# Kernel optimization log

Measured on AMD Instinct MI355X. Metric: run time of the kernel, lower is better.

Reference implementation:

```python
import jax, jax.numpy as jnp
import numpy as np

F_IN = 128
H = 512


def _uniform(key, shape, stdv):
    return jax.random.uniform(key, shape, jnp.float32, -stdv, stdv)


def setup_inputs() -> dict:
    key = jax.random.key(0)
    ks = jax.random.split(key, 20)
    B, T, F = 512, 96, F_IN
    x = jax.random.normal(ks[0], (B, T, F), jnp.float32)
    mask = jax.random.randint(ks[1], (B, T, F), 0, 2).astype(jnp.int32)
    sH = 1.0 / np.sqrt(H)
    sF = 1.0 / np.sqrt(F)
    inp = {
        'x': x,
        'mask': mask,
        # TemporalDecay h: W [H, F], b [H]
        'Wdh': _uniform(ks[2], (H, F), sH), 'bdh': _uniform(ks[3], (H,), sH),
        # TemporalDecay x (diag): W [F, F], b [F]
        'Wdx': _uniform(ks[4], (F, F), sF), 'bdx': _uniform(ks[5], (F,), sF),
        # hist_reg Linear(H, F)
        'Wh': _uniform(ks[6], (F, H), sH), 'bh': _uniform(ks[7], (F,), sH),
        # feat_reg: W [F, F] (off-diagonal mask), b [F]
        'Wf': _uniform(ks[8], (F, F), sF), 'bf': _uniform(ks[9], (F,), sF),
        # weight_combine Linear(2F, F)
        'Wc': _uniform(ks[10], (F, 2 * F), 1.0 / np.sqrt(2 * F)),
        'bc': _uniform(ks[11], (F,), 1.0 / np.sqrt(2 * F)),
        # LSTMCell(2F, H): torch gate order i, f, g, o
        'Wih': _uniform(ks[12], (4 * H, 2 * F), sH),
        'Whh': _uniform(ks[13], (4 * H, H), sH),
        'bih': _uniform(ks[14], (4 * H,), sH),
        'bhh': _uniform(ks[15], (4 * H,), sH),
    }
    return inp


def _rits_forward(x, m, Wdh, bdh, Wdx, bdx, Wh, bh, Wf, bf, Wc, bc, Wih, Whh, bih, bhh):
    B, T, F = x.shape
    eye = jnp.eye(F, dtype=x.dtype)
    Wf_m = Wf * (1.0 - eye)
    Wdx_m = Wdx * eye         # diagonal TemporalDecay

    # compute_delta (freq=1): delta[0]=0; delta[i]=m[i-1]+ (1-m[i-1])*(delta[i-1]+1)
    m_tm = jnp.swapaxes(m, 0, 1)  # [T, B, F]
    def dstep(prev, mp):
        nxt = mp + (1.0 - mp) * (prev + 1.0)
        return nxt, nxt
    _, drest = jax.lax.scan(dstep, jnp.zeros((B, F), x.dtype), m_tm[:-1])
    delta_tm = jnp.concatenate([jnp.zeros((1, B, F), x.dtype), drest], axis=0)

    x_tm = jnp.swapaxes(x, 0, 1)  # [T, B, F]

    def step(carry, inp):
        h, c = carry
        x_s, m_s, d = inp
        gamma_h = jnp.exp(-jax.nn.relu(d @ Wdh.T + bdh))          # [B, H]
        x_h = h @ Wh.T + bh                                        # [B, F]
        x_c = m_s * x_s + (1.0 - m_s) * x_h
        h = h * gamma_h
        z_h = x_c @ Wf_m.T + bf
        gamma_x = jnp.exp(-jax.nn.relu(d @ Wdx_m.T + bdx))
        alpha = jax.nn.sigmoid(jnp.concatenate([gamma_x, m_s], axis=1) @ Wc.T + bc)
        c_h = alpha * z_h + (1.0 - alpha) * x_h
        c_c = m_s * x_s + (1.0 - m_s) * c_h
        inputs = jnp.concatenate([c_c, m_s], axis=1)               # [B, 2F]
        gates = inputs @ Wih.T + bih + h @ Whh.T + bhh             # [B, 4H]
        i_g, f_g, g_g, o_g = jnp.split(gates, 4, axis=1)
        c = jax.nn.sigmoid(f_g) * c + jax.nn.sigmoid(i_g) * jnp.tanh(g_g)
        h = jax.nn.sigmoid(o_g) * jnp.tanh(c)
        return (h, c), (c_c, c_h, z_h, x_h)

    h0 = jnp.zeros((B, H), x.dtype)
    c0 = jnp.zeros((B, H), x.dtype)
    _, (c_c, c_h, z_h, x_h) = jax.lax.scan(step, (h0, c0), (x_tm, m_tm, delta_tm))
    # back to [B, T, F]
    tr = lambda a: jnp.swapaxes(a, 0, 1)
    return tr(c_c), tr(c_h), tr(z_h), tr(x_h)


def reference(x, mask, Wdh, bdh, Wdx, bdx, Wh, bh, Wf, bf, Wc, bc, Wih, Whh, bih, bhh):
    m = mask.astype(x.dtype)
    imputation, c_h, z_h, x_h = _rits_forward(
        x, m, Wdh, bdh, Wdx, bdx, Wh, bh, Wf, bf, Wc, bc, Wih, Whh, bih, bhh)
    return (imputation, (c_h, z_h, x_h))
```

## Files before the change

### kernel.cpp

```cpp
#include <hip/hip_runtime.h>
#include <cstdint>
#include <cstddef>

#define BB 512
#define TT 96
#define FF 128
#define HH 512
#define BTF 6291456
#define BH  262144

typedef unsigned short ushort_t;
typedef __attribute__((ext_vector_type(8))) short bf16x8;
typedef __attribute__((ext_vector_type(4))) float f32x4;

static constexpr size_t OFF_FLAGS = 0;
static constexpr size_t OFF_WDXD  = 2048;
static constexpr size_t OFF_DELTA = 4096;
static constexpr size_t OFF_MBF   = OFF_DELTA + 12582912;
static constexpr size_t OFF_ALPHA = OFF_MBF   + 12582912;
static constexpr size_t OFF_GH    = OFF_ALPHA + 12582912;
static constexpr size_t OFF_H     = OFF_GH    + 50331648;
static constexpr size_t OFF_HDEC  = OFF_H     + 2097152;
static constexpr size_t OFF_CCBF  = OFF_HDEC  + 1048576;

static constexpr int LDS_W     = 0;
static constexpr int LDS_GATES = 98304;
static constexpr int LDS_BIAS  = 133120;
static constexpr int LDS_XPART = 133376;
static constexpr int LDS_XC    = 141568;
static constexpr int LDS_TOTAL = 142592;

__device__ __forceinline__ float bf2f(ushort_t u) {
  union { unsigned u; float f; } c; c.u = ((unsigned)u) << 16; return c.f;
}
__device__ __forceinline__ ushort_t f2bf(float f) {
  union { float f; unsigned u; } c; c.f = f;
  unsigned x = c.u;
  unsigned r = (x + 0x7FFFu + ((x >> 16) & 1u)) >> 16;
  return (ushort_t)r;
}
__device__ __forceinline__ float lo2f(unsigned p) {
  union { unsigned u; float f; } c; c.u = p << 16; return c.f;
}
__device__ __forceinline__ float hi2f(unsigned p) {
  union { unsigned u; float f; } c; c.u = p & 0xffff0000u; return c.f;
}
__device__ __forceinline__ float sigm(float v) { return 1.0f / (1.0f + __expf(-v)); }

__device__ __forceinline__ bf16x8 cload16(const ushort_t* p) {
  union { unsigned long long q[2]; bf16x8 v; } u;
  unsigned long long* a = (unsigned long long*)p;
  u.q[0] = __hip_atomic_load(a,     __ATOMIC_RELAXED, __HIP_MEMORY_SCOPE_AGENT);
  u.q[1] = __hip_atomic_load(a + 1, __ATOMIC_RELAXED, __HIP_MEMORY_SCOPE_AGENT);
  return u.v;
}
__device__ __forceinline__ float cloadf(const float* p) {
  unsigned v = __hip_atomic_load((const unsigned*)p, __ATOMIC_RELAXED, __HIP_MEMORY_SCOPE_AGENT);
  union { unsigned u; float f; } c; c.u = v; return c.f;
}
__device__ __forceinline__ void cstore8(void* p, unsigned long long v) {
  __hip_atomic_store((unsigned long long*)p, v, __ATOMIC_RELAXED, __HIP_MEMORY_SCOPE_AGENT);
}
__device__ __forceinline__ void cstore4(void* p, unsigned v) {
  __hip_atomic_store((unsigned*)p, v, __ATOMIC_RELAXED, __HIP_MEMORY_SCOPE_AGENT);
}
__device__ __forceinline__ void cstore2(ushort_t* p, ushort_t v) {
  __hip_atomic_store(p, v, __ATOMIC_RELAXED, __HIP_MEMORY_SCOPE_AGENT);
}
__device__ __forceinline__ float rdlane_f(float v, int sl) {
  return __int_as_float(__builtin_amdgcn_readlane(__float_as_int(v), sl));
}

__global__ void k_cvt(const float* __restrict__ Wdx, char* __restrict__ ws) {
  int tid = threadIdx.x;
  unsigned* fl = (unsigned*)(ws + OFF_FLAGS);
  fl[tid] = 0; fl[256 + tid] = 0;
  float* wdxd = (float*)(ws + OFF_WDXD);
  if (tid < FF) wdxd[tid] = Wdx[tid * (FF + 1)];
}

__global__ void k_prep(const int* __restrict__ mask, char* __restrict__ ws) {
  ushort_t* delta = (ushort_t*)(ws + OFF_DELTA);
  ushort_t* mbf   = (ushort_t*)(ws + OFF_MBF);
  int gtid = blockIdx.x * 256 + threadIdx.x;
  int b = gtid >> 7, f = gtid & 127;
  const int* mrow = mask + (size_t)b * (TT * FF) + f;
  float dprev = 0.0f;
  for (int t = 0; t < TT; ++t) {
    float d;
    if (t == 0) d = 0.0f;
    else {
      int mp = mrow[(t - 1) * FF];
      d = mp ? 1.0f : dprev + 1.0f;
    }
    dprev = d;
    delta[((size_t)t * BB + b) * FF + f] = f2bf(d);
    int mc = mrow[t * FF];
    mbf[(size_t)b * (TT * FF) + t * FF + f] = f2bf((float)mc);
  }
}

__global__ __launch_bounds__(256, 4) void k_gh(const float* __restrict__ Wdh,
                                               const float* __restrict__ bdh,
                                               char* __restrict__ ws) {
  __shared__ ushort_t A_lds[64 * 136];
  __shared__ ushort_t B_lds[64 * 136];
  const ushort_t* delta = (const ushort_t*)(ws + OFF_DELTA);
  ushort_t* gh = (ushort_t*)(ws + OFF_GH);
  int tid = threadIdx.x;
  int m0 = blockIdx.x * 64;
  int n0 = blockIdx.y * 64;
  for (int v = tid; v < 1024; v += 256) {
    int row = v >> 4, seg = v & 15;
    *(uint4*)&A_lds[row * 136 + seg * 8] =
        *(const uint4*)(delta + ((size_t)(m0 + row)) * FF + seg * 8);
  }
  for (int v = tid; v < 1024; v += 256) {
    int n = v >> 4, seg = v & 15;
    const float* src = Wdh + (size_t)(n0 + n) * FF + seg * 8;
    ushort_t tmp[8];
#pragma unroll
    for (int j = 0; j < 8; ++j) tmp[j] = f2bf(src[j]);
    *(uint4*)&B_lds[n * 136 + seg * 8] = *(const uint4*)tmp;
  }
  __syncthreads();
  int wave = tid >> 6, lane = tid & 63, quad = lane >> 4, lan = lane & 15;
  int mt = wave;
  f32x4 acc[4];
#pragma unroll
  for (int nt = 0; nt < 4; ++nt) acc[nt] = (f32x4){0.f, 0.f, 0.f, 0.f};
  const ushort_t* ab = &A_lds[(mt * 16 + lan) * 136 + quad * 8];
#pragma unroll
  for (int kk = 0; kk < 4; ++kk) {
    bf16x8 af = *(const bf16x8*)(ab + kk * 32);
#pragma unroll
    for (int nt = 0; nt < 4; ++nt) {
      bf16x8 bfv = *(const bf16x8*)(&B_lds[(nt * 16 + lan) * 136 + kk * 32 + quad * 8]);
      acc[nt] = __builtin_amdgcn_mfma_f32_16x16x32_bf16(af, bfv, acc[nt], 0, 0, 0);
    }
  }
#pragma unroll
  for (int nt = 0; nt < 4; ++nt) {
#pragma unroll
    for (int r = 0; r < 4; ++r) {
      int mg = m0 + mt * 16 + quad * 4 + r;
      int nc = n0 + nt * 16 + lan;
      float v = acc[nt][r] + bdh[nc];
      gh[(size_t)mg * HH + nc] = f2bf(__expf(-fmaxf(v, 0.0f)));
    }
  }
}

__global__ __launch_bounds__(256, 4) void k_al(const float* __restrict__ Wc,
                                               const float* __restrict__ bc,
                                               const float* __restrict__ bdx,
                                               char* __restrict__ ws) {
  __shared__ ushort_t A_lds[64 * 136];
  __shared__ ushort_t B_lds[64 * 136];
  const ushort_t* delta = (const ushort_t*)(ws + OFF_DELTA);
  const ushort_t* mbf   = (const ushort_t*)(ws + OFF_MBF);
  const float* wdxd     = (const float*)(ws + OFF_WDXD);
  ushort_t* alpha = (ushort_t*)(ws + OFF_ALPHA);
  int tid = threadIdx.x;
  int m0 = blockIdx.x * 64;
  int n0 = blockIdx.y * 64;
  int wave = tid >> 6, lane = tid & 63, quad = lane >> 4, lan = lane & 15;
  int mt = wave;
  f32x4 acc[4];
#pragma unroll
  for (int nt = 0; nt < 4; ++nt) acc[nt] = (f32x4){0.f, 0.f, 0.f, 0.f};
  for (int c = 0; c < 2; ++c) {
    __syncthreads();
    if (c == 0) {
      for (int v = tid; v < 1024; v += 256) {
        int row = v >> 4, seg = v & 15;
        int mg = m0 + row;
        ushort_t tmp[8];
#pragma unroll
        for (int j = 0; j < 8; ++j) {
          int k = seg * 8 + j;
          float d = bf2f(delta[(size_t)mg * FF + k]);
          float g = __expf(-fmaxf(fmaf(d, wdxd[k], bdx[k]), 0.0f));
          tmp[j] = f2bf(g);
        }
        *(uint4*)&A_lds[row * 136 + seg * 8] = *(const uint4*)tmp;
      }
    } else {
      for (int v = tid; v < 1024; v += 256) {
        int row = v >> 4, seg = v & 15;
        int mg = m0 + row;
        int t = mg >> 9, b = mg & 511;
        *(uint4*)&A_lds[row * 136 + seg * 8] =
            *(const uint4*)(mbf + ((size_t)b * TT + t) * FF + seg * 8);
      }
    }
    for (int v = tid; v < 1024; v += 256) {
      int n = v >> 4, seg = v & 15;
      const float* src = Wc + (size_t)(n0 + n) * 256 + c * 128 + seg * 8;
      ushort_t tmp[8];
#pragma unroll
      for (int j = 0; j < 8; ++j) tmp[j] = f2bf(src[j]);
      *(uint4*)&B_lds[n * 136 + seg * 8] = *(const uint4*)tmp;
    }
    __syncthreads();
    const ushort_t* ab = &A_lds[(mt * 16 + lan) * 136 + quad * 8];
#pragma unroll
    for (int kk = 0; kk < 4; ++kk) {
      bf16x8 af = *(const bf16x8*)(ab + kk * 32);
#pragma unroll
      for (int nt = 0; nt < 4; ++nt) {
        bf16x8 bfv = *(const bf16x8*)(&B_lds[(nt * 16 + lan) * 136 + kk * 32 + quad * 8]);
        acc[nt] = __builtin_amdgcn_mfma_f32_16x16x32_bf16(af, bfv, acc[nt], 0, 0, 0);
      }
    }
  }
#pragma unroll
  for (int nt = 0; nt < 4; ++nt) {
#pragma unroll
    for (int r = 0; r < 4; ++r) {
      int mg = m0 + mt * 16 + quad * 4 + r;
      int nc = n0 + nt * 16 + lan;
      float v = acc[nt][r] + bc[nc];
      alpha[(size_t)mg * FF + nc] = f2bf(sigm(v));
    }
  }
}

__device__ __forceinline__ void bar_arrive(unsigned* cnt) {
  __syncthreads();
  if (threadIdx.x == 0)
    __hip_atomic_fetch_add(cnt, 1u, __ATOMIC_RELAXED, __HIP_MEMORY_SCOPE_AGENT);
}
__device__ __forceinline__ void bar_wait(unsigned* cnt, unsigned target) {
  if (threadIdx.x == 0) {
    while (__hip_atomic_load(cnt, __ATOMIC_RELAXED, __HIP_MEMORY_SCOPE_AGENT) < target)
      __builtin_amdgcn_s_sleep(1);
  }
  __syncthreads();
}
__device__ __forceinline__ void bar_wait_wave(unsigned* cnt, unsigned target, int lane) {
  if (lane == 0) {
    while (__hip_atomic_load(cnt, __ATOMIC_RELAXED, __HIP_MEMORY_SCOPE_AGENT) < target)
      __builtin_amdgcn_s_sleep(1);
  }
  asm volatile("" ::: "memory");
}

__global__ __launch_bounds__(512, 2) void k_main(
    const float* __restrict__ x, const int* __restrict__ mask,
    const float* __restrict__ Wh, const float* __restrict__ Wf,
    const float* __restrict__ bh, const float* __restrict__ bfr,
    const float* __restrict__ Wih, const float* __restrict__ Whh,
    const float* __restrict__ bih, const float* __restrict__ bhh,
    float* __restrict__ out, char* __restrict__ ws) {
  extern __shared__ char smem[];
  ushort_t* W_fr     = (ushort_t*)(smem + LDS_W);
  float* gates_lds   = (float*)(smem + LDS_GATES);
  float* bias_lds    = (float*)(smem + LDS_BIAS);
  float* xh_part     = (float*)(smem + LDS_XPART);
  float* xc_s        = (float*)(smem + LDS_XC);

  unsigned* cnts = (unsigned*)(ws + OFF_FLAGS);
  const ushort_t* alpha = (const ushort_t*)(ws + OFF_ALPHA);
  const ushort_t* gh    = (const ushort_t*)(ws + OFF_GH);
  const ushort_t* mbf   = (const ushort_t*)(ws + OFF_MBF);
  float*    hws  = (float*)(ws + OFF_H);
  ushort_t* hdws = (ushort_t*)(ws + OFF_HDEC);
  ushort_t* ccbf = (ushort_t*)(ws + OFF_CCBF);

  const int tid  = threadIdx.x;
  const int wg   = blockIdx.x;
  const int g    = wg & 7;
  const int mwg  = wg >> 3;
  const int ng   = mwg;
  const int wave = tid >> 6, lane = tid & 63, quad = lane >> 4, lan = lane & 15;
  const int mt = wave & 3, khalf = wave >> 2;
  const int r0 = g * 64 + mwg * 2;
  const int arow = g * 64 + mt * 16 + lan;

  unsigned* cntA = cnts + (g * 2 + 0) * 32;
  unsigned* cntB = cnts + (g * 2 + 1) * 32;

  for (int q = tid; q < 6144; q += 512) {
    int sec = q >> 10, rem = q & 1023;
    int f = rem >> 6, lw = rem & 63;
    int nt = f >> 2, kk = f & 3;
    int lan_ = lw & 15, quad_ = lw >> 4;
    int r = nt * 512 + ng * 16 + lan_;
    const float* src = (sec < 2)
        ? (Wih + (size_t)r * 256 + sec * 128 + kk * 32 + quad_ * 8)
        : (Whh + (size_t)r * 512 + (sec - 2) * 128 + kk * 32 + quad_ * 8);
    float4 v0 = *(const float4*)src;
    float4 v1 = *(const float4*)(src + 4);
    ushort_t t8[8] = { f2bf(v0.x), f2bf(v0.y), f2bf(v0.z), f2bf(v0.w),
                       f2bf(v1.x), f2bf(v1.y), f2bf(v1.z), f2bf(v1.w) };
    *(uint4*)&W_fr[q * 8] = *(const uint4*)t8;
  }
  if (tid < 64) {
    int r = (tid >> 4) * 512 + ng * 16 + (tid & 15);
    bias_lds[tid] = bih[r] + bhh[r];
  }

#define WFRAG(sec, nt, kk) (*(const bf16x8*)&W_fr[((((sec) * 16 + (nt) * 4 + (kk)) * 64 + lane)) * 8])

  unsigned wh_p[64];
  {
    const float* s0 = Wh + (size_t)lane * HH + 64 * wave;
    const float* s1 = Wh + (size_t)(lane + 64) * HH + 64 * wave;
#pragma unroll
    for (int i4 = 0; i4 < 16; ++i4) {
      float4 a = *(const float4*)(s0 + i4 * 4);
      float4 b = *(const float4*)(s1 + i4 * 4);
      wh_p[i4 * 4 + 0] = ((unsigned)f2bf(a.x)) | (((unsigned)f2bf(b.x)) << 16);
      wh_p[i4 * 4 + 1] = ((unsigned)f2bf(a.y)) | (((unsigned)f2bf(b.y)) << 16);
      wh_p[i4 * 4 + 2] = ((unsigned)f2bf(a.z)) | (((unsigned)f2bf(b.z)) << 16);
      wh_p[i4 * 4 + 3] = ((unsigned)f2bf(a.w)) | (((unsigned)f2bf(b.w)) << 16);
    }
  }
  unsigned wf_p[16];
  {
    const float* s0 = Wf + (size_t)lane * FF + 16 * wave;
    const float* s1 = Wf + (size_t)(lane + 64) * FF + 16 * wave;
#pragma unroll
    for (int i4 = 0; i4 < 4; ++i4) {
      float4 a = *(const float4*)(s0 + i4 * 4);
      float4 b = *(const float4*)(s1 + i4 * 4);
      wf_p[i4 * 4 + 0] = ((unsigned)f2bf(a.x)) | (((unsigned)f2bf(b.x)) << 16);
      wf_p[i4 * 4 + 1] = ((unsigned)f2bf(a.y)) | (((unsigned)f2bf(b.y)) << 16);
      wf_p[i4 * 4 + 2] = ((unsigned)f2bf(a.z)) | (((unsigned)f2bf(b.z)) << 16);
      wf_p[i4 * 4 + 3] = ((unsigned)f2bf(a.w)) | (((unsigned)f2bf(b.w)) << 16);
    }
  }
  const int fdot = tid & 127;
  float bh_r = 0.f, bfr_r = 0.f, wfd_r = 0.f;
  if (tid < 256) {
    bh_r  = bh[fdot];
    bfr_r = bfr[fdot];
    wfd_r = bf2f(f2bf(Wf[(size_t)fdot * FF + fdot]));
  }

  const int b_l = tid >> 3, jl0 = 2 * (tid & 7);
  const int bglob = g * 64 + b_l, j0 = ng * 16 + jl0;
  cstore8(&hws[(size_t)bglob * HH + j0], 0ull);
  cstore4(&hdws[(size_t)bglob * HH + j0], 0u);
  float c_r0 = 0.f, c_r1 = 0.f;

  unsigned epA = 0, epB = 1;
  bar_arrive(cntB);

  for (int t = 0; t < TT; ++t) {
    float xv = 0.f, mv = 0.f, al = 0.f;
    if (tid < 256) {
      int bl = tid >> 7;
      int b = r0 + bl;
      size_t gix = (size_t)b * (TT * FF) + (size_t)t * FF + fdot;
      xv = x[gix];
      mv = (float)mask[gix];
      al = bf2f(alpha[((size_t)t * BB + b) * FF + fdot]);
    }
    unsigned gh2 = 0;
    if (t < TT - 1)
      gh2 = *(const unsigned*)&gh[((size_t)(t + 1) * BB + bglob) * HH + j0];
    bf16x8 A0[4], A1[4], A2[4];
    if (khalf == 0) {
      const ushort_t* mrow = mbf + ((size_t)arow * TT + t) * FF + quad * 8;
#pragma unroll
      for (int kk = 0; kk < 4; ++kk) A0[kk] = *(const bf16x8*)(mrow + kk * 32);
    }

    bar_wait(cntB, 32u * epB);

    const float* hbuf = hws + (size_t)(t & 1) * BH;
    float h0r = cloadf(hbuf + (size_t)r0 * HH + 64 * wave + lane);
    float h1r = cloadf(hbuf + (size_t)(r0 + 1) * HH + 64 * wave + lane);
    {
      const ushort_t* hdec = hdws + (size_t)(t & 1) * BH;
      const ushort_t* hrow = hdec + (size_t)arow * HH + quad * 8;
      if (khalf == 0) {
#pragma unroll
        for (int kk = 0; kk < 4; ++kk) A1[kk] = cload16(hrow + kk * 32);
#pragma unroll
        for (int kk = 0; kk < 4; ++kk) A2[kk] = cload16(hrow + 128 + kk * 32);
      } else {
#pragma unroll
        for (int kk = 0; kk < 4; ++kk) A0[kk] = cload16(hrow + 256 + kk * 32);
#pragma unroll
        for (int kk = 0; kk < 4; ++kk) A1[kk] = cload16(hrow + 384 + kk * 32);
      }
    }

    f32x4 acc[4];
#pragma unroll
    for (int nt = 0; nt < 4; ++nt) acc[nt] = (f32x4){0.f, 0.f, 0.f, 0.f};
    if (khalf == 0) {
#pragma unroll
      for (int kk = 0; kk < 4; ++kk)
#pragma unroll
        for (int nt = 0; nt < 4; ++nt)
          acc[nt] = __builtin_amdgcn_mfma_f32_16x16x32_bf16(A0[kk], WFRAG(1, nt, kk), acc[nt], 0, 0, 0);
#pragma unroll
      for (int kk = 0; kk < 4; ++kk)
#pragma unroll
        for (int nt = 0; nt < 4; ++nt)
          acc[nt] = __builtin_amdgcn_mfma_f32_16x16x32_bf16(A1[kk], WFRAG(2, nt, kk), acc[nt], 0, 0, 0);
#pragma unroll
      for (int kk = 0; kk < 4; ++kk)
#pragma unroll
        for (int nt = 0; nt < 4; ++nt)
          acc[nt] = __builtin_amdgcn_mfma_f32_16x16x32_bf16(A2[kk], WFRAG(3, nt, kk), acc[nt], 0, 0, 0);
    } else {
#pragma unroll
      for (int kk = 0; kk < 4; ++kk)
#pragma unroll
        for (int nt = 0; nt < 4; ++nt)
          acc[nt] = __builtin_amdgcn_mfma_f32_16x16x32_bf16(A0[kk], WFRAG(4, nt, kk), acc[nt], 0, 0, 0);
#pragma unroll
      for (int kk = 0; kk < 4; ++kk)
#pragma unroll
        for (int nt = 0; nt < 4; ++nt)
          acc[nt] = __builtin_amdgcn_mfma_f32_16x16x32_bf16(A1[kk], WFRAG(5, nt, kk), acc[nt], 0, 0, 0);
#pragma unroll
      for (int nt = 0; nt < 4; ++nt)
#pragma unroll
        for (int r = 0; r < 4; ++r)
          gates_lds[(64 + mt * 16 + quad * 4 + r) * 68 + nt * 16 + lan] = acc[nt][r];
    }

    {
      float a00 = 0.f, a01 = 0.f, a10 = 0.f, a11 = 0.f;
#pragma unroll
      for (int k = 0; k < 64; ++k) {
        float hk0 = rdlane_f(h0r, k);
        float hk1 = rdlane_f(h1r, k);
        unsigned wp = wh_p[k];
        float w0 = lo2f(wp), w1 = hi2f(wp);
        a00 = fmaf(w0, hk0, a00);
        a10 = fmaf(w1, hk0, a10);
        a01 = fmaf(w0, hk1, a01);
        a11 = fmaf(w1, hk1, a11);
      }
      xh_part[(wave * 2 + 0) * 128 + lane]      = a00;
      xh_part[(wave * 2 + 0) * 128 + 64 + lane] = a10;
      xh_part[(wave * 2 + 1) * 128 + lane]      = a01;
      xh_part[(wave * 2 + 1) * 128 + 64 + lane] = a11;
    }
    __syncthreads();

    float xh_r = 0.f;
    if (tid < 256) {
      int bl = tid >> 7;
      float s = bh_r;
#pragma unroll
      for (int w2 = 0; w2 < 8; ++w2) s += xh_part[(w2 * 2 + bl) * 128 + fdot];
      xh_r = s;
      float xcv = fmaf(1.0f - mv, xh_r, mv * xv);
      xc_s[bl * 128 + fdot] = xcv;
    }
    __syncthreads();

    {
      float z00 = 0.f, z01 = 0.f, z10 = 0.f, z11 = 0.f;
      float x0 = xc_s[16 * wave + (lane & 15)];
      float x1 = xc_s[128 + 16 * wave + (lane & 15)];
#pragma unroll
      for (int k = 0; k < 16; ++k) {
        float xk0 = rdlane_f(x0, k);
        float xk1 = rdlane_f(x1, k);
        unsigned wp = wf_p[k];
        float w0 = lo2f(wp), w1 = hi2f(wp);
        z00 = fmaf(w0, xk0, z00);
        z10 = fmaf(w1, xk0, z10);
        z01 = fmaf(w0, xk1, z01);
        z11 = fmaf(w1, xk1, z11);
      }
      xh_part[(wave * 2 + 0) * 128 + lane]      = z00;
      xh_part[(wave * 2 + 0) * 128 + 64 + lane] = z10;
      xh_part[(wave * 2 + 1) * 128 + lane]      = z01;
      xh_part[(wave * 2 + 1) * 128 + 64 + lane] = z11;
    }
    __syncthreads();

    float zh = 0.f, ch = 0.f, cc = 0.f;
    if (tid < 256) {
      int bl = tid >> 7;
      int b = r0 + bl;
      float xcv = xc_s[bl * 128 + fdot];
      float s = bfr_r - xcv * wfd_r;
#pragma unroll
      for (int w2 = 0; w2 < 8; ++w2) s += xh_part[(w2 * 2 + bl) * 128 + fdot];
      zh = s;
      ch = fmaf(al, zh, (1.0f - al) * xh_r);
      cc = fmaf(1.0f - mv, ch, mv * xv);
      cstore2(&ccbf[b * FF + fdot], f2bf(cc));
    }

    bar_arrive(cntA); ++epA;

    if (tid < 256) {
      int bl = tid >> 7;
      int b = r0 + bl;
      size_t ob = (size_t)b * (TT * FF) + (size_t)t * FF + fdot;
      out[ob] = cc;
      out[BTF + ob] = ch;
      out[2 * (size_t)BTF + ob] = zh;
      out[3 * (size_t)BTF + ob] = xh_r;
    }

    if (khalf == 0) {
      bar_wait_wave(cntA, 32u * epA, lane);
      const ushort_t* ccrow = ccbf + (size_t)arow * FF + quad * 8;
      bf16x8 AC[4];
#pragma unroll
      for (int kk = 0; kk < 4; ++kk) AC[kk] = cload16(ccrow + kk * 32);
#pragma unroll
      for (int kk = 0; kk < 4; ++kk) {
#pragma unroll
        for (int nt = 0; nt < 4; ++nt) {
          acc[nt] = __builtin_amdgcn_mfma_f32_16x16x32_bf16(AC[kk], WFRAG(0, nt, kk), acc[nt], 0, 0, 0);
        }
      }
#pragma unroll
      for (int nt = 0; nt < 4; ++nt)
#pragma unroll
        for (int r = 0; r < 4; ++r)
          gates_lds[(mt * 16 + quad * 4 + r) * 68 + nt * 16 + lan] = acc[nt][r];
    }
    __syncthreads();

    {
      const float* g0 = &gates_lds[(size_t)b_l * 68 + jl0];
      const float* g1 = &gates_lds[(size_t)(64 + b_l) * 68 + jl0];
      float2 gI = make_float2(g0[0] + g1[0] + bias_lds[jl0],
                              g0[1] + g1[1] + bias_lds[jl0 + 1]);
      float2 gF = make_float2(g0[16] + g1[16] + bias_lds[16 + jl0],
                              g0[17] + g1[17] + bias_lds[16 + jl0 + 1]);
      float2 gG = make_float2(g0[32] + g1[32] + bias_lds[32 + jl0],
                              g0[33] + g1[33] + bias_lds[32 + jl0 + 1]);
      float2 gO = make_float2(g0[48] + g1[48] + bias_lds[48 + jl0],
                              g0[49] + g1[49] + bias_lds[48 + jl0 + 1]);
      c_r0 = fmaf(sigm(gF.x), c_r0, sigm(gI.x) * tanhf(gG.x));
      c_r1 = fmaf(sigm(gF.y), c_r1, sigm(gI.y) * tanhf(gG.y));
      float h0 = sigm(gO.x) * tanhf(c_r0);
      float h1 = sigm(gO.y) * tanhf(c_r1);
      float* hwN = hws + (size_t)((t + 1) & 1) * BH;
      ushort_t* hdN = hdws + (size_t)((t + 1) & 1) * BH;
      union { float2 f; unsigned long long q; } hu; hu.f = make_float2(h0, h1);
      cstore8(&hwN[(size_t)bglob * HH + j0], hu.q);
      float gHa = lo2f(gh2), gHb = hi2f(gh2);
      unsigned hp = ((unsigned)f2bf(h0 * gHa)) | (((unsigned)f2bf(h1 * gHb)) << 16);
      cstore4(&hdN[(size_t)bglob * HH + j0], hp);
    }

    bar_arrive(cntB); ++epB;
  }
#undef WFRAG
}

extern "C" void kernel_launch(void* const* d_in, const int* in_sizes, int n_in,
                              void* d_out, int out_size, void* d_ws, size_t ws_size,
                              hipStream_t stream) {
  (void)in_sizes; (void)n_in; (void)out_size; (void)ws_size;
  const float* x   = (const float*)d_in[0];
  const int*   mask= (const int*)d_in[1];
  const float* Wdh = (const float*)d_in[2];
  const float* bdh = (const float*)d_in[3];
  const float* Wdx = (const float*)d_in[4];
  const float* bdx = (const float*)d_in[5];
  const float* Wh  = (const float*)d_in[6];
  const float* bh  = (const float*)d_in[7];
  const float* Wf  = (const float*)d_in[8];
  const float* bfr = (const float*)d_in[9];
  const float* Wc  = (const float*)d_in[10];
  const float* bc  = (const float*)d_in[11];
  const float* Wih = (const float*)d_in[12];
  const float* Whh = (const float*)d_in[13];
  const float* bih = (const float*)d_in[14];
  const float* bhh = (const float*)d_in[15];
  float* out = (float*)d_out;
  char* ws = (char*)d_ws;

  hipLaunchKernelGGL(k_cvt,  dim3(1),   dim3(256), 0, stream, Wdx, ws);
  hipLaunchKernelGGL(k_prep, dim3(256), dim3(256), 0, stream, mask, ws);
  hipLaunchKernelGGL(k_gh,   dim3(768, 8), dim3(256), 0, stream, Wdh, bdh, ws);
  hipLaunchKernelGGL(k_al,   dim3(768, 2), dim3(256), 0, stream, Wc, bc, bdx, ws);

  hipFuncSetAttribute((const void*)k_main, hipFuncAttributeMaxDynamicSharedMemorySize, LDS_TOTAL);
  void* args[] = { (void*)&x, (void*)&mask, (void*)&Wh, (void*)&Wf, (void*)&bh, (void*)&bfr,
                   (void*)&Wih, (void*)&Whh, (void*)&bih, (void*)&bhh, (void*)&out, (void*)&ws };
  hipLaunchCooperativeKernel((const void*)k_main, dim3(256), dim3(512), args, LDS_TOTAL, stream);
}
```

Measured before the change: 1.516 ms.

## Map workgroup groups to XCCs and use L2-coherent sc0 loads for shared state

```diff
diff --git a/kernel.cpp b/kernel.cpp
--- a/kernel.cpp
+++ b/kernel.cpp
@@ -28,7 +28,8 @@
 static constexpr int LDS_BIAS  = 133120;
 static constexpr int LDS_XPART = 133376;
 static constexpr int LDS_XC    = 141568;
-static constexpr int LDS_TOTAL = 142592;
+static constexpr int LDS_MISC  = 142592;
+static constexpr int LDS_TOTAL = 142608;
 
 __device__ __forceinline__ float bf2f(ushort_t u) {
   union { unsigned u; float f; } c; c.u = ((unsigned)u) << 16; return c.f;
@@ -47,25 +48,19 @@
 }
 __device__ __forceinline__ float sigm(float v) { return 1.0f / (1.0f + __expf(-v)); }
 
-__device__ __forceinline__ bf16x8 cload16(const ushort_t* p) {
-  union { unsigned long long q[2]; bf16x8 v; } u;
-  unsigned long long* a = (unsigned long long*)p;
-  u.q[0] = __hip_atomic_load(a,     __ATOMIC_RELAXED, __HIP_MEMORY_SCOPE_AGENT);
-  u.q[1] = __hip_atomic_load(a + 1, __ATOMIC_RELAXED, __HIP_MEMORY_SCOPE_AGENT);
-  return u.v;
-}
-__device__ __forceinline__ float cloadf(const float* p) {
-  unsigned v = __hip_atomic_load((const unsigned*)p, __ATOMIC_RELAXED, __HIP_MEMORY_SCOPE_AGENT);
-  union { unsigned u; float f; } c; c.u = v; return c.f;
-}
-__device__ __forceinline__ void cstore8(void* p, unsigned long long v) {
-  __hip_atomic_store((unsigned long long*)p, v, __ATOMIC_RELAXED, __HIP_MEMORY_SCOPE_AGENT);
-}
-__device__ __forceinline__ void cstore4(void* p, unsigned v) {
-  __hip_atomic_store((unsigned*)p, v, __ATOMIC_RELAXED, __HIP_MEMORY_SCOPE_AGENT);
-}
-__device__ __forceinline__ void cstore2(ushort_t* p, ushort_t v) {
-  __hip_atomic_store(p, v, __ATOMIC_RELAXED, __HIP_MEMORY_SCOPE_AGENT);
+__device__ __forceinline__ bf16x8 ld16_l2(const ushort_t* p) {
+  bf16x8 r;
+  asm volatile("global_load_dwordx4 %0, %1, off sc0" : "=v"(r) : "v"(p));
+  return r;
+}
+__device__ __forceinline__ float ldf_l2(const float* p) {
+  float r;
+  asm volatile("global_load_dword %0, %1, off sc0" : "=v"(r) : "v"(p));
+  return r;
+}
+__device__ __forceinline__ void waitvm0() {
+  asm volatile("s_waitcnt vmcnt(0)" ::: "memory");
+  __builtin_amdgcn_sched_barrier(0);
 }
 __device__ __forceinline__ float rdlane_f(float v, int sl) {
   return __int_as_float(__builtin_amdgcn_readlane(__float_as_int(v), sl));
@@ -259,6 +254,7 @@
   float* bias_lds    = (float*)(smem + LDS_BIAS);
   float* xh_part     = (float*)(smem + LDS_XPART);
   float* xc_s        = (float*)(smem + LDS_XC);
+  int*   misc        = (int*)(smem + LDS_MISC);
 
   unsigned* cnts = (unsigned*)(ws + OFF_FLAGS);
   const ushort_t* alpha = (const ushort_t*)(ws + OFF_ALPHA);
@@ -268,10 +264,18 @@
   ushort_t* hdws = (ushort_t*)(ws + OFF_HDEC);
   ushort_t* ccbf = (ushort_t*)(ws + OFF_CCBF);
 
-  const int tid  = threadIdx.x;
-  const int wg   = blockIdx.x;
-  const int g    = wg & 7;
-  const int mwg  = wg >> 3;
+  const int tid = threadIdx.x;
+
+  unsigned xcc;
+  asm("s_getreg_b32 %0, hwreg(HW_REG_XCC_ID)" : "=s"(xcc));
+  const int g = (int)(xcc & 7u);
+  if (tid == 0) {
+    unsigned s = __hip_atomic_fetch_add(cnts + g * 64 + 16, 1u, __ATOMIC_RELAXED,
+                                        __HIP_MEMORY_SCOPE_AGENT);
+    misc[0] = (int)(s & 31u);
+  }
+  __syncthreads();
+  const int mwg  = misc[0];
   const int ng   = mwg;
   const int wave = tid >> 6, lane = tid & 63, quad = lane >> 4, lan = lane & 15;
   const int mt = wave & 3, khalf = wave >> 2;
@@ -341,8 +345,8 @@
 
   const int b_l = tid >> 3, jl0 = 2 * (tid & 7);
   const int bglob = g * 64 + b_l, j0 = ng * 16 + jl0;
-  cstore8(&hws[(size_t)bglob * HH + j0], 0ull);
-  cstore4(&hdws[(size_t)bglob * HH + j0], 0u);
+  *(float2*)&hws[(size_t)bglob * HH + j0] = make_float2(0.f, 0.f);
+  *(unsigned*)&hdws[(size_t)bglob * HH + j0] = 0u;
   float c_r0 = 0.f, c_r1 = 0.f;
 
   unsigned epA = 0, epB = 1;
@@ -371,23 +375,24 @@
     bar_wait(cntB, 32u * epB);
 
     const float* hbuf = hws + (size_t)(t & 1) * BH;
-    float h0r = cloadf(hbuf + (size_t)r0 * HH + 64 * wave + lane);
-    float h1r = cloadf(hbuf + (size_t)(r0 + 1) * HH + 64 * wave + lane);
+    float h0r = ldf_l2(hbuf + (size_t)r0 * HH + 64 * wave + lane);
+    float h1r = ldf_l2(hbuf + (size_t)(r0 + 1) * HH + 64 * wave + lane);
     {
       const ushort_t* hdec = hdws + (size_t)(t & 1) * BH;
       const ushort_t* hrow = hdec + (size_t)arow * HH + quad * 8;
       if (khalf == 0) {
 #pragma unroll
-        for (int kk = 0; kk < 4; ++kk) A1[kk] = cload16(hrow + kk * 32);
-#pragma unroll
-        for (int kk = 0; kk < 4; ++kk) A2[kk] = cload16(hrow + 128 + kk * 32);
+        for (int kk = 0; kk < 4; ++kk) A1[kk] = ld16_l2(hrow + kk * 32);
+#pragma unroll
+        for (int kk = 0; kk < 4; ++kk) A2[kk] = ld16_l2(hrow + 128 + kk * 32);
       } else {
 #pragma unroll
-        for (int kk = 0; kk < 4; ++kk) A0[kk] = cload16(hrow + 256 + kk * 32);
-#pragma unroll
-        for (int kk = 0; kk < 4; ++kk) A1[kk] = cload16(hrow + 384 + kk * 32);
-      }
-    }
+        for (int kk = 0; kk < 4; ++kk) A0[kk] = ld16_l2(hrow + 256 + kk * 32);
+#pragma unroll
+        for (int kk = 0; kk < 4; ++kk) A1[kk] = ld16_l2(hrow + 384 + kk * 32);
+      }
+    }
+    waitvm0();
 
     f32x4 acc[4];
 #pragma unroll
@@ -491,7 +496,7 @@
       zh = s;
       ch = fmaf(al, zh, (1.0f - al) * xh_r);
       cc = fmaf(1.0f - mv, ch, mv * xv);
-      cstore2(&ccbf[b * FF + fdot], f2bf(cc));
+      ccbf[b * FF + fdot] = f2bf(cc);
     }
 
     bar_arrive(cntA); ++epA;
@@ -511,7 +516,8 @@
       const ushort_t* ccrow = ccbf + (size_t)arow * FF + quad * 8;
       bf16x8 AC[4];
 #pragma unroll
-      for (int kk = 0; kk < 4; ++kk) AC[kk] = cload16(ccrow + kk * 32);
+      for (int kk = 0; kk < 4; ++kk) AC[kk] = ld16_l2(ccrow + kk * 32);
+      waitvm0();
 #pragma unroll
       for (int kk = 0; kk < 4; ++kk) {
 #pragma unroll
@@ -544,11 +550,10 @@
       float h1 = sigm(gO.y) * tanhf(c_r1);
       float* hwN = hws + (size_t)((t + 1) & 1) * BH;
       ushort_t* hdN = hdws + (size_t)((t + 1) & 1) * BH;
-      union { float2 f; unsigned long long q; } hu; hu.f = make_float2(h0, h1);
-      cstore8(&hwN[(size_t)bglob * HH + j0], hu.q);
+      *(float2*)&hwN[(size_t)bglob * HH + j0] = make_float2(h0, h1);
       float gHa = lo2f(gh2), gHb = hi2f(gh2);
       unsigned hp = ((unsigned)f2bf(h0 * gHa)) | (((unsigned)f2bf(h1 * gHb)) << 16);
-      cstore4(&hdN[(size_t)bglob * HH + j0], hp);
+      *(unsigned*)&hdN[(size_t)bglob * HH + j0] = hp;
     }
 
     bar_arrive(cntB); ++epB;
```

New measurement: 1.356 ms. -10.6%, faster.
